# Optimization experiments

Measured on AMD Instinct MI355X. Metric: run time of the kernel, lower is better.

Reference implementation:

```python
import jax, jax.numpy as jnp
import numpy as np

BATCH, DIM, LAYER_NUM = 16384, 1024, 3

def setup_inputs() -> dict:
    key = jax.random.key(0)
    k1, k2 = jax.random.split(key)
    x = jax.random.normal(k1, (BATCH, DIM), dtype=jnp.float32)
    # glorot_normal for shape (dim, 1): std = sqrt(2/(dim+1))
    kernels = jax.random.normal(k2, (LAYER_NUM, DIM), dtype=jnp.float32) * np.sqrt(2.0 / (DIM + 1)).astype(np.float32)
    bias = jnp.zeros((LAYER_NUM, DIM), dtype=jnp.float32)
    return {"x": x, "kernels": kernels, "bias": bias}

def reference(x, kernels, bias):
    # CrossNet: x_{l+1} = x_0 * (x_l^T w_l) + x_l + b_l
    # The original builds (B, dim, dim) = x_0 x_l^T then contracts with w_l (dim,1);
    # by associativity this equals x_0 * (x_l . w_l) — identical math, O(dim) work.
    x0 = x
    xl = x
    for i in range(kernels.shape[0]):
        s = jnp.einsum('bd,d->b', xl, kernels[i])  # (B,) scalar x_l^T w
        xl = x0 * s[:, None] + xl + bias[i][None, :]
    return xl
```

## Files before the change

kernel.cpp:

```cpp
#include <hip/hip_runtime.h>


#define CN_BATCH 16384
#define CN_DIM   1024
#define CN_LAYERS 3

typedef float f32x4 __attribute__((ext_vector_type(4)));

__global__ __launch_bounds__(256) void crossnet_kernel(
    const float* __restrict__ x,
    const float* __restrict__ kernels,
    const float* __restrict__ bias,
    float* __restrict__ out)
{
    const int wave = threadIdx.x >> 6;
    const int lane = threadIdx.x & 63;
    const int pair = (blockIdx.x << 2) + wave;
    const int rowA = pair * 2;
    const int rowB = rowA + 1;

    const float* xrowA = x + (size_t)rowA * CN_DIM;
    const float* xrowB = x + (size_t)rowB * CN_DIM;

    f32x4 x0A[4], xlA[4], x0B[4], xlB[4];
#pragma unroll
    for (int j = 0; j < 4; ++j) {
        x0A[j] = *reinterpret_cast<const f32x4*>(xrowA + j * 256 + lane * 4);
        x0B[j] = *reinterpret_cast<const f32x4*>(xrowB + j * 256 + lane * 4);
    }
#pragma unroll
    for (int j = 0; j < 4; ++j) { xlA[j] = x0A[j]; xlB[j] = x0B[j]; }

#pragma unroll
    for (int i = 0; i < CN_LAYERS; ++i) {
        const float* krow = kernels + i * CN_DIM;
        const float* brow = bias    + i * CN_DIM;

        float pA = 0.0f, pB = 0.0f;
#pragma unroll
        for (int j = 0; j < 4; ++j) {
            f32x4 k = *reinterpret_cast<const f32x4*>(krow + j * 256 + lane * 4);
            pA = fmaf(xlA[j].x, k.x, pA);  pB = fmaf(xlB[j].x, k.x, pB);
            pA = fmaf(xlA[j].y, k.y, pA);  pB = fmaf(xlB[j].y, k.y, pB);
            pA = fmaf(xlA[j].z, k.z, pA);  pB = fmaf(xlB[j].z, k.z, pB);
            pA = fmaf(xlA[j].w, k.w, pA);  pB = fmaf(xlB[j].w, k.w, pB);
        }
#pragma unroll
        for (int off = 32; off >= 1; off >>= 1) {
            pA += __shfl_xor(pA, off, 64);
            pB += __shfl_xor(pB, off, 64);
        }
        const float sA = pA, sB = pB;

#pragma unroll
        for (int j = 0; j < 4; ++j) {
            f32x4 b = *reinterpret_cast<const f32x4*>(brow + j * 256 + lane * 4);
            xlA[j].x = fmaf(x0A[j].x, sA, xlA[j].x) + b.x;
            xlA[j].y = fmaf(x0A[j].y, sA, xlA[j].y) + b.y;
            xlA[j].z = fmaf(x0A[j].z, sA, xlA[j].z) + b.z;
            xlA[j].w = fmaf(x0A[j].w, sA, xlA[j].w) + b.w;
            xlB[j].x = fmaf(x0B[j].x, sB, xlB[j].x) + b.x;
            xlB[j].y = fmaf(x0B[j].y, sB, xlB[j].y) + b.y;
            xlB[j].z = fmaf(x0B[j].z, sB, xlB[j].z) + b.z;
            xlB[j].w = fmaf(x0B[j].w, sB, xlB[j].w) + b.w;
        }
    }

    float* orowA = out + (size_t)rowA * CN_DIM;
    float* orowB = out + (size_t)rowB * CN_DIM;
#pragma unroll
    for (int j = 0; j < 4; ++j) {
        *reinterpret_cast<f32x4*>(orowA + j * 256 + lane * 4) = xlA[j];
        *reinterpret_cast<f32x4*>(orowB + j * 256 + lane * 4) = xlB[j];
    }
}

extern "C" void kernel_launch(void* const* d_in, const int* in_sizes, int n_in,
                              void* d_out, int out_size, void* d_ws, size_t ws_size,
                              hipStream_t stream) {
    const float* x       = (const float*)d_in[0];
    const float* kernels = (const float*)d_in[1];
    const float* bias    = (const float*)d_in[2];
    float* out           = (float*)d_out;

    dim3 grid(CN_BATCH / 8);
    dim3 block(256);
    crossnet_kernel<<<grid, block, 0, stream>>>(x, kernels, bias, out);
}
```

Measured before the change: 25.99 us.

## Collapse three cross layers into one closed-form scale with single reduction pass

Rewrites the recurrence algebraically: every x_l equals x0 scaled by a per-row factor plus an accumulated bias. All dot products (x0·w_i and bias·w terms) are computed in one pass, with one merged shuffle-reduction phase instead of three serialized ones. Output stores become nontemporal. This removes the serial dependency between layers at the cost of more live registers and a different floating-point summation order.

After: 24.90 us (median of 2 runs). 1.04x faster.

```diff
diff --git a/kernel.cpp b/kernel.cpp
--- a/kernel.cpp
+++ b/kernel.cpp
@@ -3,7 +3,6 @@
 
 #define CN_BATCH 16384
 #define CN_DIM   1024
-#define CN_LAYERS 3
 
 typedef float f32x4 __attribute__((ext_vector_type(4)));
 
@@ -17,61 +16,90 @@
     const int lane = threadIdx.x & 63;
     const int pair = (blockIdx.x << 2) + wave;
     const int rowA = pair * 2;
-    const int rowB = rowA + 1;
+    const int eoff = lane * 4;
 
     const float* xrowA = x + (size_t)rowA * CN_DIM;
-    const float* xrowB = x + (size_t)rowB * CN_DIM;
+    const float* xrowB = xrowA + CN_DIM;
 
-    f32x4 x0A[4], xlA[4], x0B[4], xlB[4];
+    const float* k1 = kernels;
+    const float* k2 = kernels + CN_DIM;
+    const float* k3 = kernels + 2 * CN_DIM;
+    const float* b1 = bias;
+    const float* b2 = bias + CN_DIM;
+    const float* b3 = bias + 2 * CN_DIM;
+
+    f32x4 x0A[4], x0B[4];
 #pragma unroll
     for (int j = 0; j < 4; ++j) {
-        x0A[j] = *reinterpret_cast<const f32x4*>(xrowA + j * 256 + lane * 4);
-        x0B[j] = *reinterpret_cast<const f32x4*>(xrowB + j * 256 + lane * 4);
+        x0A[j] = *reinterpret_cast<const f32x4*>(xrowA + j * 256 + eoff);
+        x0B[j] = *reinterpret_cast<const f32x4*>(xrowB + j * 256 + eoff);
     }
+
+    float a1A = 0.f, a2A = 0.f, a3A = 0.f;
+    float a1B = 0.f, a2B = 0.f, a3B = 0.f;
+    float c2  = 0.f, c3  = 0.f;
+    f32x4 Bs[4];
 #pragma unroll
-    for (int j = 0; j < 4; ++j) { xlA[j] = x0A[j]; xlB[j] = x0B[j]; }
-
+    for (int j = 0; j < 4; ++j) {
+        f32x4 vk1 = *reinterpret_cast<const f32x4*>(k1 + j * 256 + eoff);
+        f32x4 vk2 = *reinterpret_cast<const f32x4*>(k2 + j * 256 + eoff);
+        f32x4 vk3 = *reinterpret_cast<const f32x4*>(k3 + j * 256 + eoff);
+        f32x4 vb1 = *reinterpret_cast<const f32x4*>(b1 + j * 256 + eoff);
+        f32x4 vb2 = *reinterpret_cast<const f32x4*>(b2 + j * 256 + eoff);
+        f32x4 vb3 = *reinterpret_cast<const f32x4*>(b3 + j * 256 + eoff);
+        f32x4 b12 = vb1 + vb2;
+        Bs[j] = b12 + vb3;
 #pragma unroll
-    for (int i = 0; i < CN_LAYERS; ++i) {
-        const float* krow = kernels + i * CN_DIM;
-        const float* brow = bias    + i * CN_DIM;
-
-        float pA = 0.0f, pB = 0.0f;
-#pragma unroll
-        for (int j = 0; j < 4; ++j) {
-            f32x4 k = *reinterpret_cast<const f32x4*>(krow + j * 256 + lane * 4);
-            pA = fmaf(xlA[j].x, k.x, pA);  pB = fmaf(xlB[j].x, k.x, pB);
-            pA = fmaf(xlA[j].y, k.y, pA);  pB = fmaf(xlB[j].y, k.y, pB);
-            pA = fmaf(xlA[j].z, k.z, pA);  pB = fmaf(xlB[j].z, k.z, pB);
-            pA = fmaf(xlA[j].w, k.w, pA);  pB = fmaf(xlB[j].w, k.w, pB);
-        }
-#pragma unroll
-        for (int off = 32; off >= 1; off >>= 1) {
-            pA += __shfl_xor(pA, off, 64);
-            pB += __shfl_xor(pB, off, 64);
-        }
-        const float sA = pA, sB = pB;
-
-#pragma unroll
-        for (int j = 0; j < 4; ++j) {
-            f32x4 b = *reinterpret_cast<const f32x4*>(brow + j * 256 + lane * 4);
-            xlA[j].x = fmaf(x0A[j].x, sA, xlA[j].x) + b.x;
-            xlA[j].y = fmaf(x0A[j].y, sA, xlA[j].y) + b.y;
-            xlA[j].z = fmaf(x0A[j].z, sA, xlA[j].z) + b.z;
-            xlA[j].w = fmaf(x0A[j].w, sA, xlA[j].w) + b.w;
-            xlB[j].x = fmaf(x0B[j].x, sB, xlB[j].x) + b.x;
-            xlB[j].y = fmaf(x0B[j].y, sB, xlB[j].y) + b.y;
-            xlB[j].z = fmaf(x0B[j].z, sB, xlB[j].z) + b.z;
-            xlB[j].w = fmaf(x0B[j].w, sB, xlB[j].w) + b.w;
+        for (int c = 0; c < 4; ++c) {
+            a1A = fmaf(x0A[j][c], vk1[c], a1A);
+            a2A = fmaf(x0A[j][c], vk2[c], a2A);
+            a3A = fmaf(x0A[j][c], vk3[c], a3A);
+            a1B = fmaf(x0B[j][c], vk1[c], a1B);
+            a2B = fmaf(x0B[j][c], vk2[c], a2B);
+            a3B = fmaf(x0B[j][c], vk3[c], a3B);
+            c2  = fmaf(vb1[c],    vk2[c], c2);
+            c3  = fmaf(b12[c],    vk3[c], c3);
         }
     }
 
+#pragma unroll
+    for (int o = 32; o >= 1; o >>= 1) {
+        a1A += __shfl_xor(a1A, o, 64);
+        a2A += __shfl_xor(a2A, o, 64);
+        a3A += __shfl_xor(a3A, o, 64);
+        a1B += __shfl_xor(a1B, o, 64);
+        a2B += __shfl_xor(a2B, o, 64);
+        a3B += __shfl_xor(a3B, o, 64);
+        c2  += __shfl_xor(c2,  o, 64);
+        c3  += __shfl_xor(c3,  o, 64);
+    }
+
+    const float t1A = 1.0f + a1A;
+    const float s2A = fmaf(t1A, a2A, c2);
+    const float t2A = t1A + s2A;
+    const float s3A = fmaf(t2A, a3A, c3);
+    const float t3A = t2A + s3A;
+
+    const float t1B = 1.0f + a1B;
+    const float s2B = fmaf(t1B, a2B, c2);
+    const float t2B = t1B + s2B;
+    const float s3B = fmaf(t2B, a3B, c3);
+    const float t3B = t2B + s3B;
+
     float* orowA = out + (size_t)rowA * CN_DIM;
-    float* orowB = out + (size_t)rowB * CN_DIM;
+    float* orowB = orowA + CN_DIM;
 #pragma unroll
     for (int j = 0; j < 4; ++j) {
-        *reinterpret_cast<f32x4*>(orowA + j * 256 + lane * 4) = xlA[j];
-        *reinterpret_cast<f32x4*>(orowB + j * 256 + lane * 4) = xlB[j];
+        f32x4 oA, oB;
+#pragma unroll
+        for (int c = 0; c < 4; ++c) {
+            oA[c] = fmaf(x0A[j][c], t3A, Bs[j][c]);
+            oB[c] = fmaf(x0B[j][c], t3B, Bs[j][c]);
+        }
+        __builtin_nontemporal_store(oA,
+            reinterpret_cast<f32x4*>(orowA + j * 256 + eoff));
+        __builtin_nontemporal_store(oB,
+            reinterpret_cast<f32x4*>(orowB + j * 256 + eoff));
     }
 }
 
```
